# Optimization experiments

Measured on AMD Instinct MI355X. Metric: run time of the kernel, lower is better.

Reference implementation:

```python
import jax, jax.numpy as jnp
import numpy as np

N_EMBD = 1024
D_K = 1024
D_V = 1024

def setup_inputs() -> dict:
    key = jax.random.key(0)
    k1, k2, k3, k4 = jax.random.split(key, 4)
    B, T = 4, 2048
    std = N_EMBD ** -0.5
    x = jax.random.normal(k1, (B, T, N_EMBD), dtype=jnp.float32)
    Wq = jax.random.normal(k2, (N_EMBD, D_K), dtype=jnp.float32) * std
    Wk = jax.random.normal(k3, (N_EMBD, D_K), dtype=jnp.float32) * std
    Wv = jax.random.normal(k4, (N_EMBD, D_V), dtype=jnp.float32) * std
    return {"x": x, "Wq": Wq, "Wk": Wk, "Wv": Wv}

def reference(x, Wq, Wk, Wv):
    # x: [B, T, C]
    T = x.shape[1]
    q = x @ Wq  # [B, T, d_k]
    k = x @ Wk  # [B, T, d_k]
    v = x @ Wv  # [B, T, d_v]
    scale = Wk.shape[1] ** -0.5
    wei = jnp.einsum('btd,bsd->bts', q, k) * scale  # [B, T, T]
    causal = jnp.tril(jnp.ones((T, T), dtype=bool))
    wei = jnp.where(causal, wei, -jnp.inf)
    wei = jax.nn.softmax(wei, axis=-1)
    return wei @ v  # [B, T, d_v]
```

## Files before the change

### kernel.cpp

```cpp
#include <hip/hip_runtime.h>
#include <hip/hip_bf16.h>
#include <stdint.h>

using bf16_t = __hip_bfloat16;
typedef __bf16 bf16x8 __attribute__((ext_vector_type(8)));
typedef float f32x4 __attribute__((ext_vector_type(4)));

__device__ __forceinline__ void async_lds16(const void* g, void* l) {
  __builtin_amdgcn_global_load_lds(
      (const __attribute__((address_space(1))) void*)g,
      (__attribute__((address_space(3))) void*)l, 16, 0, 0);
}

__device__ __forceinline__ unsigned short f2bf_u16(float f) {
  __hip_bfloat16 h = __float2bfloat16(f);
  return __builtin_bit_cast(unsigned short, h);
}

__device__ __forceinline__ float bf2f(unsigned short u) {
  __hip_bfloat16 h = __builtin_bit_cast(__hip_bfloat16, u);
  return __bfloat162float(h);
}

__global__ __launch_bounds__(256) void convert_all_kernel(
    const float* __restrict__ x, bf16_t* __restrict__ xb,
    const float* __restrict__ Wq, const float* __restrict__ Wk,
    const float* __restrict__ Wv, bf16_t* __restrict__ wt) {
  __shared__ bf16_t tile[32][33];
  const int bid = blockIdx.x;
  if (bid < 8192) {
    size_t i = ((size_t)bid * 256 + threadIdx.x) * 4;
    float4 v = *(const float4*)(x + i);
    ushort4 o;
    o.x = f2bf_u16(v.x);
    o.y = f2bf_u16(v.y);
    o.z = f2bf_u16(v.z);
    o.w = f2bf_u16(v.w);
    *(ushort4*)(xb + i) = o;
    return;
  }
  const int w = bid - 8192;
  const int z = w >> 10;
  const int bxy = w & 1023;
  const float* W = (z == 0) ? Wq : (z == 1) ? Wk : Wv;
  bf16_t* WT = wt + (size_t)z * 1024 * 1024;
  const int tx = threadIdx.x & 31;
  const int ty = threadIdx.x >> 5;
  const int bx = bxy & 31;
  const int by = bxy >> 5;
  const int k0 = by * 32, n0 = bx * 32;
#pragma unroll
  for (int j = 0; j < 32; j += 8)
    tile[ty + j][tx] = __float2bfloat16(W[(size_t)(k0 + ty + j) * 1024 + n0 + tx]);
  __syncthreads();
#pragma unroll
  for (int j = 0; j < 32; j += 8)
    WT[(size_t)(n0 + ty + j) * 1024 + k0 + tx] = tile[tx][ty + j];
}

template <int OUT_MODE>
__global__ __launch_bounds__(512, 2) void gemm_pipe_kernel(
    const bf16_t* __restrict__ A, const bf16_t* __restrict__ BT,
    void* __restrict__ Cv, void* __restrict__ Cv2, void* __restrict__ Cv3,
    int M, int N, int K, int lda, int ldb) {
  int bx = blockIdx.x, by = blockIdx.y;
  {
    const int gx = gridDim.x;
    const int nwg = gx * gridDim.y;
    const int id = by * gx + bx;
    const int cpx = nwg >> 3;
    const int swz = (id & 7) * cpx + (id >> 3);
    by = swz / gx;
    bx = swz % gx;
  }
  const int m0 = by * 128;
  const int n0 = bx * 256;
  const int nkt = K >> 5;

  __shared__ bf16_t lsA[3 * 128 * 32];
  __shared__ bf16_t lsB[3 * 256 * 32];

  const int tid = threadIdx.x;
  const int wid = tid >> 6;
  const int lane = tid & 63;
  const int wm = wid >> 2;
  const int wn = wid & 3;

  const int sr = tid >> 2;
  const int ss = tid & 3;
  const int sswz = ss ^ ((sr >> 1) & 3);
  const bf16_t* gA = A + (size_t)(m0 + sr) * lda + sswz * 8;
  const bf16_t* gB0 = BT + (size_t)(n0 + sr) * ldb + sswz * 8;
  const bf16_t* gB1 = BT + (size_t)(n0 + 128 + sr) * ldb + sswz * 8;

  const int kslot = (lane >> 4) ^ ((lane >> 1) & 3);
  const int abase = (wm * 64 + (lane & 15)) * 32 + kslot * 8;
  const int bbase = (wn * 64 + (lane & 15)) * 32 + kslot * 8;

  f32x4 acc[4][4];
  const f32x4 zero = {0.f, 0.f, 0.f, 0.f};
#pragma unroll
  for (int m = 0; m < 4; ++m)
#pragma unroll
    for (int n = 0; n < 4; ++n) acc[m][n] = zero;

  async_lds16(gA, lsA + wid * 512);
  async_lds16(gB0, lsB + wid * 512);
  async_lds16(gB1, lsB + 4096 + wid * 512);
  if (nkt > 1) {
    async_lds16(gA + 32, lsA + 4096 + wid * 512);
    async_lds16(gB0 + 32, lsB + 8192 + wid * 512);
    async_lds16(gB1 + 32, lsB + 8192 + 4096 + wid * 512);
    asm volatile("s_waitcnt vmcnt(3)" ::: "memory");
  } else {
    asm volatile("s_waitcnt vmcnt(0)" ::: "memory");
  }
  __builtin_amdgcn_s_barrier();

  int cb = 0;
  for (int t = 0; t < nkt; ++t) {
    const bf16_t* bufA = lsA + cb * 4096;
    const bf16_t* bufB = lsB + cb * 8192;
    int sb = cb + 2;
    if (sb >= 3) sb -= 3;

    bf16x8 af[4], bfr[4];
#pragma unroll
    for (int mf = 0; mf < 4; ++mf)
      af[mf] = *(const bf16x8*)(bufA + abase + mf * 512);
    bfr[0] = *(const bf16x8*)(bufB + bbase);
    bfr[1] = *(const bf16x8*)(bufB + bbase + 512);
    if (t + 2 < nkt) {
      async_lds16(gA + (t + 2) * 32, lsA + sb * 4096 + wid * 512);
      async_lds16(gB0 + (t + 2) * 32, lsB + sb * 8192 + wid * 512);
    }
    __builtin_amdgcn_s_barrier();
    __builtin_amdgcn_s_setprio(1);
#pragma unroll
    for (int mf = 0; mf < 4; ++mf)
#pragma unroll
      for (int nf = 0; nf < 2; ++nf)
        acc[mf][nf] = __builtin_amdgcn_mfma_f32_16x16x32_bf16(
            af[mf], bfr[nf], acc[mf][nf], 0, 0, 0);
    __builtin_amdgcn_s_setprio(0);
    __builtin_amdgcn_s_barrier();

    bfr[2] = *(const bf16x8*)(bufB + bbase + 1024);
    bfr[3] = *(const bf16x8*)(bufB + bbase + 1536);
    if (t + 2 < nkt)
      async_lds16(gB1 + (t + 2) * 32, lsB + sb * 8192 + 4096 + wid * 512);
    if (t + 2 < nkt) {
      asm volatile("s_waitcnt vmcnt(3)" ::: "memory");
    } else if (t + 2 == nkt) {
      asm volatile("s_waitcnt vmcnt(0)" ::: "memory");
    }
    __builtin_amdgcn_s_barrier();
    __builtin_amdgcn_s_setprio(1);
#pragma unroll
    for (int mf = 0; mf < 4; ++mf)
#pragma unroll
      for (int nf = 2; nf < 4; ++nf)
        acc[mf][nf] = __builtin_amdgcn_mfma_f32_16x16x32_bf16(
            af[mf], bfr[nf], acc[mf][nf], 0, 0, 0);
    __builtin_amdgcn_s_setprio(0);
    __builtin_amdgcn_s_barrier();

    cb = cb + 1;
    if (cb >= 3) cb -= 3;
  }

  const int erow = wm * 64 + (lane >> 4) * 4;
  const int ecol = wn * 64 + (lane & 15);
  if (n0 < 2048) {
    bf16_t* C = (bf16_t*)((n0 < 1024) ? Cv : Cv2);
    const int cb0 = n0 & 1023;
#pragma unroll
    for (int m = 0; m < 4; ++m)
#pragma unroll
      for (int n = 0; n < 4; ++n)
#pragma unroll
        for (int j = 0; j < 4; ++j) {
          int r = m0 + erow + m * 16 + j;
          int c = cb0 + ecol + n * 16;
          C[(size_t)r * 1024 + c] = __float2bfloat16(acc[m][n][j]);
        }
  } else {
    bf16_t* C = (bf16_t*)Cv3;
    const int d0 = n0 - 2048;
#pragma unroll
    for (int m = 0; m < 4; ++m)
#pragma unroll
      for (int n = 0; n < 4; ++n)
#pragma unroll
        for (int j = 0; j < 4; ++j) {
          int r = m0 + erow + m * 16 + j;
          int d = d0 + ecol + n * 16;
          int b = r >> 11, tt = r & 2047;
          C[((size_t)b * 1024 + d) * 2048 + tt] = __float2bfloat16(acc[m][n][j]);
        }
  }
}

template <int OUT_MODE, bool CAUSAL_SKIP, bool PAIRED>
__global__ __launch_bounds__(512, 2) void gemm128_kernel(
    const bf16_t* __restrict__ A, const bf16_t* __restrict__ BT,
    void* __restrict__ Cv, int K, int lda, int ldb, int ldc,
    long long aBatch, long long bBatch, long long cBatch) {
  const int bx = blockIdx.x, by = blockIdx.y;
  if (CAUSAL_SKIP && bx > by) return;
  const bf16_t* Ab = A + (size_t)blockIdx.z * aBatch;
  const bf16_t* Bb = BT + (size_t)blockIdx.z * bBatch;

  __shared__ bf16_t lsA[3 * 4096];
  __shared__ bf16_t lsB[3 * 4096];

  const int tid = threadIdx.x;
  const int wid = tid >> 6;
  const int lane = tid & 63;
  const int wm = wid >> 2;
  const int wn = wid & 3;

  const int sr = tid >> 2;
  const int sswz = (tid & 3) ^ ((sr >> 1) & 3);
  const int n0 = bx * 128;
  const bf16_t* gB = Bb + (size_t)(n0 + sr) * ldb + sswz * 8;

  const int kslot = (lane >> 4) ^ ((lane >> 1) & 3);
  const int aRd = (wm * 64 + (lane & 15)) * 32 + kslot * 8;
  const int bRd = (wn * 32 + (lane & 15)) * 32 + kslot * 8;

  const int njobs = PAIRED ? 2 : 1;
  for (int job = 0; job < njobs; ++job) {
    const int byE = (PAIRED && job) ? (15 - by) : by;
    const int m0 = byE * 128;
    int nkt = K >> 5;
    if (PAIRED) {
      int lim = (m0 + 128) >> 5;
      nkt = nkt < lim ? nkt : lim;
    }
    const bf16_t* gA = Ab + (size_t)(m0 + sr) * lda + sswz * 8;

    f32x4 acc[4][2];
    const f32x4 zero = {0.f, 0.f, 0.f, 0.f};
#pragma unroll
    for (int m = 0; m < 4; ++m)
#pragma unroll
      for (int n = 0; n < 2; ++n) acc[m][n] = zero;

    async_lds16(gA, lsA + wid * 512);
    async_lds16(gB, lsB + wid * 512);
    if (nkt > 1) {
      async_lds16(gA + 32, lsA + 4096 + wid * 512);
      async_lds16(gB + 32, lsB + 4096 + wid * 512);
      asm volatile("s_waitcnt vmcnt(2)" ::: "memory");
    } else {
      asm volatile("s_waitcnt vmcnt(0)" ::: "memory");
    }
    __builtin_amdgcn_s_barrier();

    int cb = 0;
    for (int t = 0; t < nkt; ++t) {
      const bf16_t* bufA = lsA + cb * 4096;
      const bf16_t* bufB = lsB + cb * 4096;
      int sb = cb + 2;
      if (sb >= 3) sb -= 3;

      bf16x8 af[4], bfr[2];
#pragma unroll
      for (int mf = 0; mf < 4; ++mf)
        af[mf] = *(const bf16x8*)(bufA + aRd + mf * 512);
      bfr[0] = *(const bf16x8*)(bufB + bRd);
      bfr[1] = *(const bf16x8*)(bufB + bRd + 512);
      if (t + 2 < nkt) {
        async_lds16(gA + (t + 2) * 32, lsA + sb * 4096 + wid * 512);
        async_lds16(gB + (t + 2) * 32, lsB + sb * 4096 + wid * 512);
        asm volatile("s_waitcnt vmcnt(2)" ::: "memory");
      } else if (t + 2 == nkt) {
        asm volatile("s_waitcnt vmcnt(0)" ::: "memory");
      }
      __builtin_amdgcn_s_barrier();
      __builtin_amdgcn_s_setprio(1);
#pragma unroll
      for (int mf = 0; mf < 4; ++mf)
#pragma unroll
        for (int nf = 0; nf < 2; ++nf)
          acc[mf][nf] = __builtin_amdgcn_mfma_f32_16x16x32_bf16(
              af[mf], bfr[nf], acc[mf][nf], 0, 0, 0);
      __builtin_amdgcn_s_setprio(0);
      __builtin_amdgcn_s_barrier();

      cb = cb + 1;
      if (cb >= 3) cb -= 3;
    }

    const int erow = wm * 64 + (lane >> 4) * 4;
    const int ecol = wn * 32 + (lane & 15);
    if (OUT_MODE == 2) {
      float* C = (float*)Cv + (size_t)blockIdx.z * cBatch;
#pragma unroll
      for (int m = 0; m < 4; ++m)
#pragma unroll
        for (int n = 0; n < 2; ++n)
#pragma unroll
          for (int j = 0; j < 4; ++j) {
            int r = m0 + erow + m * 16 + j;
            int c = n0 + ecol + n * 16;
            C[(size_t)r * ldc + c] = acc[m][n][j];
          }
    } else {
      bf16_t* C = (bf16_t*)Cv + (size_t)blockIdx.z * cBatch;
#pragma unroll
      for (int m = 0; m < 4; ++m)
#pragma unroll
        for (int n = 0; n < 2; ++n)
#pragma unroll
          for (int j = 0; j < 4; ++j) {
            int r = m0 + erow + m * 16 + j;
            int c = n0 + ecol + n * 16;
            C[(size_t)r * ldc + c] = __float2bfloat16(acc[m][n][j]);
          }
    }
  }
}

__global__ __launch_bounds__(256) void softmax_causal_kernel(bf16_t* __restrict__ Sb) {
  const int lane = threadIdx.x & 63;
  const int rg = blockIdx.x * 4 + (threadIdx.x >> 6);
  const int b = rg >> 11;
  const int t = rg & 2047;
  bf16_t* srow = Sb + (size_t)b * 8388608 + (size_t)t * 4096;
  const int qmax = t >> 8;

  float v[8][4];
#pragma unroll
  for (int it = 0; it < 8; ++it) {
    if (it <= qmax) {
      ushort4 u = *(const ushort4*)(srow + (it * 64 + lane) * 4);
      v[it][0] = bf2f(u.x);
      v[it][1] = bf2f(u.y);
      v[it][2] = bf2f(u.z);
      v[it][3] = bf2f(u.w);
    } else {
      v[it][0] = v[it][1] = v[it][2] = v[it][3] = 0.f;
    }
  }

  float mx = -3.0e38f;
#pragma unroll
  for (int it = 0; it < 8; ++it) {
    int s0 = (it * 64 + lane) * 4;
    if (s0 + 0 <= t) mx = fmaxf(mx, v[it][0]);
    if (s0 + 1 <= t) mx = fmaxf(mx, v[it][1]);
    if (s0 + 2 <= t) mx = fmaxf(mx, v[it][2]);
    if (s0 + 3 <= t) mx = fmaxf(mx, v[it][3]);
  }
#pragma unroll
  for (int off = 32; off > 0; off >>= 1) mx = fmaxf(mx, __shfl_xor(mx, off, 64));

  const float kMul = 0.03125f * 1.4426950408889634f;
  float p[8][4];
  float sum = 0.f;
#pragma unroll
  for (int it = 0; it < 8; ++it) {
    int s0 = (it * 64 + lane) * 4;
    float e0 = (s0 + 0 <= t) ? exp2f((v[it][0] - mx) * kMul) : 0.f;
    float e1 = (s0 + 1 <= t) ? exp2f((v[it][1] - mx) * kMul) : 0.f;
    float e2 = (s0 + 2 <= t) ? exp2f((v[it][2] - mx) * kMul) : 0.f;
    float e3 = (s0 + 3 <= t) ? exp2f((v[it][3] - mx) * kMul) : 0.f;
    p[it][0] = e0; p[it][1] = e1; p[it][2] = e2; p[it][3] = e3;
    sum += (e0 + e1) + (e2 + e3);
  }
#pragma unroll
  for (int off = 32; off > 0; off >>= 1) sum += __shfl_xor(sum, off, 64);
  const float inv = 1.f / sum;

#pragma unroll
  for (int it = 0; it < 8; ++it) {
    if (it <= qmax) {
      ushort4 o;
      o.x = f2bf_u16(p[it][0] * inv);
      o.y = f2bf_u16(p[it][1] * inv);
      o.z = f2bf_u16(p[it][2] * inv);
      o.w = f2bf_u16(p[it][3] * inv);
      *(ushort4*)(srow + (it * 64 + lane) * 4) = o;
    }
  }
}

extern "C" void kernel_launch(void* const* d_in, const int* in_sizes, int n_in,
                              void* d_out, int out_size, void* d_ws, size_t ws_size,
                              hipStream_t stream) {
  (void)in_sizes; (void)n_in; (void)out_size;
  const float* x = (const float*)d_in[0];
  const float* Wq = (const float*)d_in[1];
  const float* Wk = (const float*)d_in[2];
  const float* Wv = (const float*)d_in[3];
  float* out = (float*)d_out;

  char* ws = (char*)d_ws;
  const size_t NEED = 123731968;
  const bool batched = ws_size >= NEED;

  bf16_t* xb = (bf16_t*)ws;
  bf16_t* Sb;
  bf16_t *WT, *Qb, *Kb, *VT;
  if (batched) {
    Sb = (bf16_t*)ws;
    WT = (bf16_t*)(ws + 67108864);
    Qb = (bf16_t*)(ws + 73400320);
    Kb = (bf16_t*)(ws + 90177536);
    VT = (bf16_t*)(ws + 106954752);
  } else {
    Sb = (bf16_t*)ws;
    WT = (bf16_t*)(ws + 16777216);
    Qb = (bf16_t*)(ws + 16777216 + 6291456);
    Kb = Qb + 8388608;
    VT = Kb + 8388608;
  }

  convert_all_kernel<<<11264, 256, 0, stream>>>(x, xb, Wq, Wk, Wv, WT);

  gemm_pipe_kernel<3><<<dim3(12, 64, 1), 512, 0, stream>>>(
      xb, WT, Qb, Kb, VT, 8192, 3072, 1024, 1024, 1024);

  const int nbat = batched ? 4 : 1;
  for (int pass = 0; pass < (batched ? 1 : 4); ++pass) {
    const size_t qoff = (size_t)pass * 2048 * 1024;
    const bf16_t* Qp = Qb + qoff;
    const bf16_t* Kp = Kb + qoff;
    const bf16_t* Vp = VT + qoff;
    float* op = out + qoff;
    gemm128_kernel<5, true, false><<<dim3(16, 16, nbat), 512, 0, stream>>>(
        Qp, Kp, Sb, 1024, 1024, 1024, 4096,
        batched ? 2097152LL : 0, batched ? 2097152LL : 0,
        batched ? 8388608LL : 0);
    softmax_causal_kernel<<<batched ? 2048 : 512, 256, 0, stream>>>(Sb);
    gemm128_kernel<2, false, true><<<dim3(8, 8, nbat), 512, 0, stream>>>(
        Sb, Vp, op, 2048, 4096, 2048, 1024,
        batched ? 8388608LL : 0, batched ? 2097152LL : 0,
        batched ? 2097152LL : 0);
  }
}
```

Baseline: 174.8 us.

## Replace triple-buffered split-phase projection GEMM loop with simple double buffering

The projection GEMM drops its three-stage LDS ring, where each K step was split into two half-MFMA phases with four barriers and partial vmcnt waits. It now uses a two-buffer scheme: it prefetches the next tile, runs all 16 MFMAs, waits for all loads, and takes one barrier per iteration. This removes barrier and bookkeeping overhead and cuts LDS use. In exchange the prefetch distance shrinks to one tile, so global-load latency is less hidden. The kernel is also renamed and its unused M/N arguments removed.

Measured after the change: 177.4 us. No clear change (+1.5%).

```diff
diff --git a/kernel.cpp b/kernel.cpp
--- a/kernel.cpp
+++ b/kernel.cpp
@@ -59,10 +59,10 @@
 }
 
 template <int OUT_MODE>
-__global__ __launch_bounds__(512, 2) void gemm_pipe_kernel(
+__global__ __launch_bounds__(512, 2) void gemm_proj_kernel(
     const bf16_t* __restrict__ A, const bf16_t* __restrict__ BT,
     void* __restrict__ Cv, void* __restrict__ Cv2, void* __restrict__ Cv3,
-    int M, int N, int K, int lda, int ldb) {
+    int K, int lda, int ldb) {
   int bx = blockIdx.x, by = blockIdx.y;
   {
     const int gx = gridDim.x;
@@ -77,8 +77,8 @@
   const int n0 = bx * 256;
   const int nkt = K >> 5;
 
-  __shared__ bf16_t lsA[3 * 128 * 32];
-  __shared__ bf16_t lsB[3 * 256 * 32];
+  __shared__ bf16_t lsA[2 * 4096];
+  __shared__ bf16_t lsB[2 * 8192];
 
   const int tid = threadIdx.x;
   const int wid = tid >> 6;
@@ -87,8 +87,7 @@
   const int wn = wid & 3;
 
   const int sr = tid >> 2;
-  const int ss = tid & 3;
-  const int sswz = ss ^ ((sr >> 1) & 3);
+  const int sswz = (tid & 3) ^ ((sr >> 1) & 3);
   const bf16_t* gA = A + (size_t)(m0 + sr) * lda + sswz * 8;
   const bf16_t* gB0 = BT + (size_t)(n0 + sr) * ldb + sswz * 8;
   const bf16_t* gB1 = BT + (size_t)(n0 + 128 + sr) * ldb + sswz * 8;
@@ -97,6 +96,16 @@
   const int abase = (wm * 64 + (lane & 15)) * 32 + kslot * 8;
   const int bbase = (wn * 64 + (lane & 15)) * 32 + kslot * 8;
 
+  auto stage = [&](int t) {
+    const int buf = t & 1;
+    bf16_t* dA = lsA + buf * 4096 + wid * 512;
+    bf16_t* dB = lsB + buf * 8192 + wid * 512;
+    const size_t co = (size_t)t * 32;
+    async_lds16(gA + co, dA);
+    async_lds16(gB0 + co, dB);
+    async_lds16(gB1 + co, dB + 4096);
+  };
+
   f32x4 acc[4][4];
   const f32x4 zero = {0.f, 0.f, 0.f, 0.f};
 #pragma unroll
@@ -104,69 +113,36 @@
 #pragma unroll
     for (int n = 0; n < 4; ++n) acc[m][n] = zero;
 
-  async_lds16(gA, lsA + wid * 512);
-  async_lds16(gB0, lsB + wid * 512);
-  async_lds16(gB1, lsB + 4096 + wid * 512);
-  if (nkt > 1) {
-    async_lds16(gA + 32, lsA + 4096 + wid * 512);
-    async_lds16(gB0 + 32, lsB + 8192 + wid * 512);
-    async_lds16(gB1 + 32, lsB + 8192 + 4096 + wid * 512);
-    asm volatile("s_waitcnt vmcnt(3)" ::: "memory");
-  } else {
-    asm volatile("s_waitcnt vmcnt(0)" ::: "memory");
-  }
+  stage(0);
+  asm volatile("s_waitcnt vmcnt(0)" ::: "memory");
   __builtin_amdgcn_s_barrier();
 
-  int cb = 0;
   for (int t = 0; t < nkt; ++t) {
-    const bf16_t* bufA = lsA + cb * 4096;
-    const bf16_t* bufB = lsB + cb * 8192;
-    int sb = cb + 2;
-    if (sb >= 3) sb -= 3;
+    const bf16_t* bufA = lsA + (t & 1) * 4096;
+    const bf16_t* bufB = lsB + (t & 1) * 8192;
+    if (t + 1 < nkt) stage(t + 1);
 
     bf16x8 af[4], bfr[4];
 #pragma unroll
     for (int mf = 0; mf < 4; ++mf)
       af[mf] = *(const bf16x8*)(bufA + abase + mf * 512);
-    bfr[0] = *(const bf16x8*)(bufB + bbase);
-    bfr[1] = *(const bf16x8*)(bufB + bbase + 512);
-    if (t + 2 < nkt) {
-      async_lds16(gA + (t + 2) * 32, lsA + sb * 4096 + wid * 512);
-      async_lds16(gB0 + (t + 2) * 32, lsB + sb * 8192 + wid * 512);
-    }
-    __builtin_amdgcn_s_barrier();
+#pragma unroll
+    for (int nf = 0; nf < 4; ++nf)
+      bfr[nf] = *(const bf16x8*)(bufB + bbase + nf * 512);
+
     __builtin_amdgcn_s_setprio(1);
 #pragma unroll
     for (int mf = 0; mf < 4; ++mf)
 #pragma unroll
-      for (int nf = 0; nf < 2; ++nf)
+      for (int nf = 0; nf < 4; ++nf)
         acc[mf][nf] = __builtin_amdgcn_mfma_f32_16x16x32_bf16(
             af[mf], bfr[nf], acc[mf][nf], 0, 0, 0);
     __builtin_amdgcn_s_setprio(0);
+
+    if (t + 1 < nkt) {
+      asm volatile("s_waitcnt vmcnt(0)" ::: "memory");
+    }
     __builtin_amdgcn_s_barrier();
-
-    bfr[2] = *(const bf16x8*)(bufB + bbase + 1024);
-    bfr[3] = *(const bf16x8*)(bufB + bbase + 1536);
-    if (t + 2 < nkt)
-      async_lds16(gB1 + (t + 2) * 32, lsB + sb * 8192 + 4096 + wid * 512);
-    if (t + 2 < nkt) {
-      asm volatile("s_waitcnt vmcnt(3)" ::: "memory");
-    } else if (t + 2 == nkt) {
-      asm volatile("s_waitcnt vmcnt(0)" ::: "memory");
-    }
-    __builtin_amdgcn_s_barrier();
-    __builtin_amdgcn_s_setprio(1);
-#pragma unroll
-    for (int mf = 0; mf < 4; ++mf)
-#pragma unroll
-      for (int nf = 2; nf < 4; ++nf)
-        acc[mf][nf] = __builtin_amdgcn_mfma_f32_16x16x32_bf16(
-            af[mf], bfr[nf], acc[mf][nf], 0, 0, 0);
-    __builtin_amdgcn_s_setprio(0);
-    __builtin_amdgcn_s_barrier();
-
-    cb = cb + 1;
-    if (cb >= 3) cb -= 3;
   }
 
   const int erow = wm * 64 + (lane >> 4) * 4;
@@ -420,8 +396,8 @@
 
   convert_all_kernel<<<11264, 256, 0, stream>>>(x, xb, Wq, Wk, Wv, WT);
 
-  gemm_pipe_kernel<3><<<dim3(12, 64, 1), 512, 0, stream>>>(
-      xb, WT, Qb, Kb, VT, 8192, 3072, 1024, 1024, 1024);
+  gemm_proj_kernel<3><<<dim3(12, 64, 1), 512, 0, stream>>>(
+      xb, WT, Qb, Kb, VT, 1024, 1024, 1024);
 
   const int nbat = batched ? 4 : 1;
   for (int pass = 0; pass < (batched ? 1 : 4); ++pass) {
```
